# Performance work log

Measured on AMD Instinct MI355X. Metric: run time of the kernel, lower is better.

## Reference

```python
import jax, jax.numpy as jnp
import numpy as np

D_MODEL = 1024
NUM_HEADS = 16
HEAD_DIM = D_MODEL // NUM_HEADS


def setup_inputs() -> dict:
    key = jax.random.key(0)
    ks = jax.random.split(key, 9)
    B, S = 4, 2048
    scale = 1.0 / np.sqrt(D_MODEL)
    x = jax.random.normal(ks[0], (B, S, D_MODEL), dtype=jnp.float32)
    Wq = jax.random.normal(ks[1], (D_MODEL, D_MODEL), dtype=jnp.float32) * scale
    bq = jnp.zeros((D_MODEL,), dtype=jnp.float32)
    Wk = jax.random.normal(ks[2], (D_MODEL, D_MODEL), dtype=jnp.float32) * scale
    bk = jnp.zeros((D_MODEL,), dtype=jnp.float32)
    Wv = jax.random.normal(ks[3], (D_MODEL, D_MODEL), dtype=jnp.float32) * scale
    bv = jnp.zeros((D_MODEL,), dtype=jnp.float32)
    Wo = jax.random.normal(ks[4], (D_MODEL, D_MODEL), dtype=jnp.float32) * scale
    bo = jnp.zeros((D_MODEL,), dtype=jnp.float32)
    return {"x": x, "Wq": Wq, "bq": bq, "Wk": Wk, "bk": bk,
            "Wv": Wv, "bv": bv, "Wo": Wo, "bo": bo}


def reference(x, Wq, bq, Wk, bk, Wv, bv, Wo, bo):
    B, S, D = x.shape
    H, Hd = NUM_HEADS, HEAD_DIM
    # linear projections then split heads: [B,S,D] -> [B,H,S,Hd]
    def split(t):
        return t.reshape(B, S, H, Hd).transpose(0, 2, 1, 3)
    q = split(x @ Wq + bq)
    k = split(x @ Wk + bk)
    v = split(x @ Wv + bv)
    scores = jnp.einsum('bhsd,bhtd->bhst', q, k) / jnp.sqrt(
        jnp.asarray(Hd, dtype=jnp.float32))
    attn = jax.nn.softmax(scores, axis=-1)
    out = jnp.einsum('bhst,bhtd->bhsd', attn, v)  # [B,H,S,Hd]
    out = out.transpose(0, 2, 1, 3).reshape(B, S, D)
    return out @ Wo + bo
```

## Files before the change

kernel.cpp:

```cpp
#include <hip/hip_runtime.h>

#define DM 1024
#define NH 16
#define HD 64
#define SEQ 2048
#define BATCH 4
#define MROWS (BATCH*SEQ)

typedef short short8 __attribute__((ext_vector_type(8)));
typedef float f32x4 __attribute__((ext_vector_type(4)));
typedef unsigned short u16x8 __attribute__((ext_vector_type(8)));
typedef unsigned short u16x4 __attribute__((ext_vector_type(4)));

__device__ inline unsigned short f2b(float f) {
    union { float f; unsigned u; } v; v.f = f;
    unsigned r = v.u + 0x7fffu + ((v.u >> 16) & 1u);
    return (unsigned short)(r >> 16);
}

__device__ inline void gload_lds16(const void* g, void* l) {
    __builtin_amdgcn_global_load_lds(
        (const __attribute__((address_space(1))) void*)g,
        (__attribute__((address_space(3))) void*)l, 16, 0, 0);
}

__device__ inline unsigned cvt_pk_bf16(float lo, float hi) {
    unsigned r;
    asm("v_cvt_pk_bf16_f32 %0, %1, %2" : "=v"(r) : "v"(lo), "v"(hi));
    return r;
}

__global__ void k_cvt_x(const float* __restrict__ x, unsigned short* __restrict__ xb) {
    long i = ((long)blockIdx.x * 256 + threadIdx.x) * 8;
    float4 a = *reinterpret_cast<const float4*>(x + i);
    float4 b = *reinterpret_cast<const float4*>(x + i + 4);
    u16x8 o;
    o[0]=f2b(a.x); o[1]=f2b(a.y); o[2]=f2b(a.z); o[3]=f2b(a.w);
    o[4]=f2b(b.x); o[5]=f2b(b.y); o[6]=f2b(b.z); o[7]=f2b(b.w);
    *reinterpret_cast<u16x8*>(xb + i) = o;
}

__global__ void k_cvt_wT(const float* W0, const float* W1, const float* W2, const float* W3,
                         unsigned short* __restrict__ out) {
    const float* Ws[4] = {W0, W1, W2, W3};
    const float* W = Ws[blockIdx.z];
    unsigned short* o = out + (size_t)blockIdx.z * DM * DM;
    __shared__ float t[64][65];
    int tx = threadIdx.x & 15, ty = threadIdx.x >> 4;
    int nb = blockIdx.x * 64, kb = blockIdx.y * 64;
#pragma unroll
    for (int i = 0; i < 4; ++i) {
        int r = ty + 16 * i;
        float4 v = *reinterpret_cast<const float4*>(W + (size_t)(kb + r) * DM + nb + tx * 4);
        t[r][tx*4+0] = v.x; t[r][tx*4+1] = v.y; t[r][tx*4+2] = v.z; t[r][tx*4+3] = v.w;
    }
    __syncthreads();
#pragma unroll
    for (int i = 0; i < 4; ++i) {
        int r = ty + 16 * i;
        u16x4 pv;
#pragma unroll
        for (int j = 0; j < 4; ++j) pv[j] = f2b(t[tx*4+j][r]);
        *reinterpret_cast<u16x4*>(o + (size_t)(nb + r) * DM + kb + tx * 4) = pv;
    }
}

#define BM 128
#define BN 128
#define BK 64
#define QSCALE 0.1803368801f

__global__ __launch_bounds__(256) void k_gemm_qkv(const unsigned short* __restrict__ A,
                                                  const unsigned short* __restrict__ WT,
                                                  const float* __restrict__ bq,
                                                  const float* __restrict__ bk,
                                                  const float* __restrict__ bv,
                                                  unsigned short* __restrict__ Qb,
                                                  unsigned short* __restrict__ Kb,
                                                  unsigned short* __restrict__ VTb) {
    __shared__ unsigned short lds[BM*BK + BN*BK];
    unsigned short* lA = lds;
    unsigned short* lB = lds + BM*BK;
    int tid = threadIdx.x, lane = tid & 63, wv = tid >> 6;
    int wr = wv >> 1, wc = wv & 1;
    int c = lane & 15, g = lane >> 4;
    int m0 = blockIdx.x * BM, n0 = blockIdx.y * BN;
    f32x4 acc[4][4] = {};

    for (int kt = 0; kt < DM / BK; ++kt) {
#pragma unroll
        for (int it = 0; it < 4; ++it) {
            int sgi = it * 256 + tid;
            int row = sgi >> 3, blk = sgi & 7;
            int srcoff = kt * BK + ((blk ^ (row & 7)) << 3);
            gload_lds16(A  + (size_t)(m0 + row) * DM + srcoff, &lA[(it*256 + wv*64) * 8]);
            gload_lds16(WT + (size_t)(n0 + row) * DM + srcoff, &lB[(it*256 + wv*64) * 8]);
        }
        __syncthreads();
#pragma unroll
        for (int ks = 0; ks < 2; ++ks) {
            short8 af[4], bf[4];
#pragma unroll
            for (int mi = 0; mi < 4; ++mi) {
                int row = wr*64 + mi*16 + c;
                af[mi] = *reinterpret_cast<const short8*>(&lA[row*64 + (((ks*4 + g) ^ (row & 7)) << 3)]);
            }
#pragma unroll
            for (int ni = 0; ni < 4; ++ni) {
                int row = wc*64 + ni*16 + c;
                bf[ni] = *reinterpret_cast<const short8*>(&lB[row*64 + (((ks*4 + g) ^ (row & 7)) << 3)]);
            }
#pragma unroll
            for (int mi = 0; mi < 4; ++mi)
#pragma unroll
                for (int ni = 0; ni < 4; ++ni)
                    acc[mi][ni] = __builtin_amdgcn_mfma_f32_16x16x32_bf16(af[mi], bf[ni], acc[mi][ni], 0, 0, 0);
        }
        __syncthreads();
    }

    int mat = n0 >> 10;
    int gb = n0 & 1023;
    const float* bias = (mat == 0) ? bq : (mat == 1) ? bk : bv;

    if (mat < 2) {
        unsigned short* outb = (mat == 0) ? Qb : Kb;
        float sc = (mat == 0) ? QSCALE : 1.0f;
#pragma unroll
        for (int mi = 0; mi < 4; ++mi)
#pragma unroll
            for (int ni = 0; ni < 4; ++ni)
#pragma unroll
                for (int r = 0; r < 4; ++r) {
                    int gr = m0 + wr*64 + mi*16 + 4*g + r;
                    int gc = gb + wc*64 + ni*16 + c;
                    float v = (acc[mi][ni][r] + bias[gc]) * sc;
                    int b = gr >> 11, s = gr & 2047, h = gc >> 6, d = gc & 63;
                    outb[(((size_t)(b*NH + h) * SEQ + s) << 6) + d] = f2b(v);
                }
    } else {
        unsigned short* t = lds;
#pragma unroll
        for (int mi = 0; mi < 4; ++mi)
#pragma unroll
            for (int ni = 0; ni < 4; ++ni)
#pragma unroll
                for (int r = 0; r < 4; ++r) {
                    int lr = wr*64 + mi*16 + 4*g + r;
                    int lc = wc*64 + ni*16 + c;
                    t[lc*128 + lr] = f2b(acc[mi][ni][r] + bias[gb + lc]);
                }
        __syncthreads();
#pragma unroll
        for (int i = 0; i < 8; ++i) {
            int idx = (i*256 + tid) * 8;
            int lc = idx >> 7, lr = idx & 127;
            int gcol = gb + lc, grow = m0 + lr;
            int b = grow >> 11, s = grow & 2047, h = gcol >> 6, d = gcol & 63;
            *reinterpret_cast<u16x8*>(&VTb[((size_t)((b*NH + h) << 6) + d) * SEQ + s]) =
                *reinterpret_cast<u16x8*>(&t[idx]);
        }
    }
}

__global__ __launch_bounds__(256) void k_gemm_o(const unsigned short* __restrict__ A,
                                                const unsigned short* __restrict__ Bt,
                                                const float* __restrict__ bias,
                                                float* __restrict__ outf) {
    __shared__ unsigned short lds[BM*BK + BN*BK];
    unsigned short* lA = lds;
    unsigned short* lB = lds + BM*BK;
    int tid = threadIdx.x, lane = tid & 63, wv = tid >> 6;
    int wr = wv >> 1, wc = wv & 1;
    int c = lane & 15, g = lane >> 4;
    int m0 = blockIdx.x * BM, n0 = blockIdx.y * BN;
    f32x4 acc[4][4] = {};

    for (int kt = 0; kt < DM / BK; ++kt) {
#pragma unroll
        for (int it = 0; it < 4; ++it) {
            int sgi = it * 256 + tid;
            int row = sgi >> 3, blk = sgi & 7;
            int srcoff = kt * BK + ((blk ^ (row & 7)) << 3);
            gload_lds16(A  + (size_t)(m0 + row) * DM + srcoff, &lA[(it*256 + wv*64) * 8]);
            gload_lds16(Bt + (size_t)(n0 + row) * DM + srcoff, &lB[(it*256 + wv*64) * 8]);
        }
        __syncthreads();
#pragma unroll
        for (int ks = 0; ks < 2; ++ks) {
            short8 af[4], bf[4];
#pragma unroll
            for (int mi = 0; mi < 4; ++mi) {
                int row = wr*64 + mi*16 + c;
                af[mi] = *reinterpret_cast<const short8*>(&lA[row*64 + (((ks*4 + g) ^ (row & 7)) << 3)]);
            }
#pragma unroll
            for (int ni = 0; ni < 4; ++ni) {
                int row = wc*64 + ni*16 + c;
                bf[ni] = *reinterpret_cast<const short8*>(&lB[row*64 + (((ks*4 + g) ^ (row & 7)) << 3)]);
            }
#pragma unroll
            for (int mi = 0; mi < 4; ++mi)
#pragma unroll
                for (int ni = 0; ni < 4; ++ni)
                    acc[mi][ni] = __builtin_amdgcn_mfma_f32_16x16x32_bf16(af[mi], bf[ni], acc[mi][ni], 0, 0, 0);
        }
        __syncthreads();
    }

#pragma unroll
    for (int mi = 0; mi < 4; ++mi)
#pragma unroll
        for (int ni = 0; ni < 4; ++ni)
#pragma unroll
            for (int r = 0; r < 4; ++r) {
                int gr = m0 + wr*64 + mi*16 + 4*g + r;
                int gc = n0 + wc*64 + ni*16 + c;
                outf[(size_t)gr * DM + gc] = acc[mi][ni][r] + bias[gc];
            }
}

__global__ __launch_bounds__(256) void k_attn(const unsigned short* __restrict__ Q,
                                              const unsigned short* __restrict__ K,
                                              const unsigned short* __restrict__ VT,
                                              unsigned short* __restrict__ AO) {
    __shared__ unsigned short kt[2][64*64], vt[2][64*64];
    int tid = threadIdx.x, lane = tid & 63, wv = tid >> 6;
    int c = lane & 15, g = lane >> 4;

    int flat = blockIdx.x;
    int nb = (flat & 7) * 256 + (flat >> 3);
    int qb = nb & 31, bh = nb >> 5;

    const unsigned short* Qh = Q  + (size_t)bh * SEQ * HD;
    const unsigned short* Kh = K  + (size_t)bh * SEQ * HD;
    const unsigned short* Vh = VT + (size_t)bh * HD * SEQ;

    int qrow = qb*64 + wv*16 + c;
    short8 qf0 = *reinterpret_cast<const short8*>(&Qh[(size_t)qrow*HD +      g*8]);
    short8 qf1 = *reinterpret_cast<const short8*>(&Qh[(size_t)qrow*HD + 32 + g*8]);

    int row = tid >> 3, blk = tid & 7;
    int xo = (blk ^ (row & 7)) << 3;
    auto srowf = [](int r) {
        return ((r >> 4) & 1)*32 + ((r >> 2) & 3)*8 + ((r >> 5) & 1)*4 + (r & 3);
    };
    const unsigned short* gK0 = Kh + (size_t)srowf(row)      * HD + xo;
    const unsigned short* gK1 = Kh + (size_t)srowf(row + 32) * HD + xo;
    const unsigned short* gV0 = Vh + (size_t)row        * SEQ + xo;
    const unsigned short* gV1 = Vh + (size_t)(row + 32) * SEQ + xo;
    unsigned ldso = wv * 512;

    int swz0 = (g ^ (c & 7)) << 3;
    int swz1 = ((4 + g) ^ (c & 7)) << 3;
    const unsigned short* kb0 = &kt[0][c*64 + swz0];
    const unsigned short* kb1 = &kt[0][c*64 + swz1];
    const unsigned short* vb0 = &vt[0][c*64 + swz0];
    const unsigned short* vb1 = &vt[0][c*64 + swz1];

    float m = -1e30f;
    f32x4 oacc[4] = {}, lacc = {};
    const short ob = (short)0x3F80;
    const short8 ones = {ob, ob, ob, ob, ob, ob, ob, ob};

#define STAGE(SB) do {                                                        \
        gload_lds16(gK0, &kt[SB][ldso]);                                      \
        gload_lds16(gK1, &kt[SB][2048 + ldso]);                               \
        gload_lds16(gV0, &vt[SB][ldso]);                                      \
        gload_lds16(gV1, &vt[SB][2048 + ldso]);                               \
        gK0 += 64*HD; gK1 += 64*HD; gV0 += 64; gV1 += 64;                     \
    } while (0)

#define TILE(BUFO, PRE) do {                                                  \
        PRE;                                                                  \
        f32x4 sacc[4] = {};                                                   \
        __builtin_amdgcn_s_setprio(1);                                        \
        _Pragma("unroll")                                                     \
        for (int nt = 0; nt < 4; ++nt) {                                      \
            short8 kf0 = *reinterpret_cast<const short8*>(kb0 + (BUFO) + nt*1024); \
            short8 kf1 = *reinterpret_cast<const short8*>(kb1 + (BUFO) + nt*1024); \
            sacc[nt] = __builtin_amdgcn_mfma_f32_16x16x32_bf16(kf0, qf0, sacc[nt], 0, 0, 0); \
            sacc[nt] = __builtin_amdgcn_mfma_f32_16x16x32_bf16(kf1, qf1, sacc[nt], 0, 0, 0); \
        }                                                                     \
        __builtin_amdgcn_s_setprio(0);                                        \
        float x0 = fmaxf(fmaxf(sacc[0][0], sacc[0][1]), sacc[0][2]);          \
        float x1 = fmaxf(fmaxf(sacc[0][3], sacc[1][0]), sacc[1][1]);          \
        float x2 = fmaxf(fmaxf(sacc[1][2], sacc[1][3]), sacc[2][0]);          \
        float x3 = fmaxf(fmaxf(sacc[2][1], sacc[2][2]), sacc[2][3]);          \
        float x4 = fmaxf(fmaxf(sacc[3][0], sacc[3][1]), sacc[3][2]);          \
        float tm = fmaxf(fmaxf(fmaxf(x0, x1), fmaxf(x2, x3)), fmaxf(x4, sacc[3][3])); \
        if (__any(tm > m + 8.0f)) {                                           \
            tm = fmaxf(tm, __shfl_xor(tm, 16, 64));                           \
            tm = fmaxf(tm, __shfl_xor(tm, 32, 64));                           \
            float mn = fmaxf(m, tm);                                          \
            float corr = __builtin_amdgcn_exp2f(m - mn);                      \
            m = mn; lacc *= corr;                                             \
            _Pragma("unroll")                                                 \
            for (int ft = 0; ft < 4; ++ft)                                    \
                _Pragma("unroll")                                             \
                for (int r = 0; r < 4; ++r) oacc[ft][r] *= corr;              \
        }                                                                     \
        _Pragma("unroll")                                                     \
        for (int nt = 0; nt < 4; ++nt)                                        \
            _Pragma("unroll")                                                 \
            for (int r = 0; r < 4; ++r)                                       \
                sacc[nt][r] = __builtin_amdgcn_exp2f(sacc[nt][r] - m);        \
        union { unsigned u[4]; short8 v; } U0, U1;                            \
        U0.u[0] = cvt_pk_bf16(sacc[0][0], sacc[0][1]);                        \
        U0.u[1] = cvt_pk_bf16(sacc[0][2], sacc[0][3]);                        \
        U0.u[2] = cvt_pk_bf16(sacc[2][0], sacc[2][1]);                        \
        U0.u[3] = cvt_pk_bf16(sacc[2][2], sacc[2][3]);                        \
        U1.u[0] = cvt_pk_bf16(sacc[1][0], sacc[1][1]);                        \
        U1.u[1] = cvt_pk_bf16(sacc[1][2], sacc[1][3]);                        \
        U1.u[2] = cvt_pk_bf16(sacc[3][0], sacc[3][1]);                        \
        U1.u[3] = cvt_pk_bf16(sacc[3][2], sacc[3][3]);                        \
        short8 pa0 = U0.v, pa1 = U1.v;                                        \
        __builtin_amdgcn_s_setprio(1);                                        \
        _Pragma("unroll")                                                     \
        for (int ft = 0; ft < 4; ++ft) {                                      \
            short8 vf0 = *reinterpret_cast<const short8*>(vb0 + (BUFO) + ft*1024); \
            short8 vf1 = *reinterpret_cast<const short8*>(vb1 + (BUFO) + ft*1024); \
            oacc[ft] = __builtin_amdgcn_mfma_f32_16x16x32_bf16(vf0, pa0, oacc[ft], 0, 0, 0); \
            oacc[ft] = __builtin_amdgcn_mfma_f32_16x16x32_bf16(vf1, pa1, oacc[ft], 0, 0, 0); \
        }                                                                     \
        lacc = __builtin_amdgcn_mfma_f32_16x16x32_bf16(ones, pa0, lacc, 0, 0, 0); \
        lacc = __builtin_amdgcn_mfma_f32_16x16x32_bf16(ones, pa1, lacc, 0, 0, 0); \
        __builtin_amdgcn_s_setprio(0);                                        \
        __syncthreads();                                                      \
    } while (0)

    STAGE(0);
    __syncthreads();

    for (int tp = 0; tp < 15; ++tp) {
        TILE(0,    STAGE(1));
        TILE(4096, STAGE(0));
    }
    TILE(0,    STAGE(1));
    TILE(4096, (void)0);

#undef STAGE
#undef TILE

    int b = bh >> 4, h = bh & 15;
    float inv = 1.f / lacc[0];
#pragma unroll
    for (int ft = 0; ft < 4; ++ft) {
        u16x4 o4;
#pragma unroll
        for (int r = 0; r < 4; ++r) o4[r] = f2b(oacc[ft][r] * inv);
        *reinterpret_cast<u16x4*>(
            &AO[(size_t)(b*SEQ + qrow) * DM + h*HD + ft*16 + 4*g]) = o4;
    }
}

extern "C" void kernel_launch(void* const* d_in, const int* in_sizes, int n_in,
                              void* d_out, int out_size, void* d_ws, size_t ws_size,
                              hipStream_t stream) {
    const float* x  = (const float*)d_in[0];
    const float* Wq = (const float*)d_in[1];
    const float* bq = (const float*)d_in[2];
    const float* Wk = (const float*)d_in[3];
    const float* bk = (const float*)d_in[4];
    const float* Wv = (const float*)d_in[5];
    const float* bv = (const float*)d_in[6];
    const float* Wo = (const float*)d_in[7];
    const float* bo = (const float*)d_in[8];

    char* ws = (char*)d_ws;
    unsigned short* xb  = (unsigned short*)(ws);
    unsigned short* wT  = (unsigned short*)(ws + (16u<<20));
    unsigned short* Qb  = (unsigned short*)(ws + (24u<<20));
    unsigned short* Kb  = (unsigned short*)(ws + (40u<<20));
    unsigned short* VTb = (unsigned short*)(ws + (56u<<20));
    unsigned short* AOb = (unsigned short*)(ws + (72u<<20));

    k_cvt_x<<<dim3(MROWS*DM/8/256), 256, 0, stream>>>(x, xb);
    k_cvt_wT<<<dim3(16,16,4), 256, 0, stream>>>(Wq, Wk, Wv, Wo, wT);

    k_gemm_qkv<<<dim3(MROWS/BM, 3*DM/BN), 256, 0, stream>>>(xb, wT, bq, bk, bv, Qb, Kb, VTb);

    k_attn<<<dim3(SEQ/64 * BATCH*NH), 256, 0, stream>>>(Qb, Kb, VTb, AOb);

    k_gemm_o<<<dim3(MROWS/BM, DM/BN), 256, 0, stream>>>(AOb, wT + 3*DM*DM, bo, (float*)d_out);
}
```

Measured before the change: 199.6 us.

## Switch attention to 32x32x16 MFMA with 128-query blocks per workgroup

Rewrites the attention kernel to use 32x32x16 bf16 MFMAs, so each wave handles 32 query rows and the workgroup covers 128 queries. This halves the number of workgroups and the K/V tile loads per query. The P fragment for the PV MFMA is built with v_permlane32_swap, and the K staging drops the old row permutation in favour of an XOR-swizzled direct layout. In exchange it uses more accumulator registers per wave, which may cut occupancy, and relies on tricky fragment-layout correctness.

```diff
diff --git a/kernel.cpp b/kernel.cpp
--- a/kernel.cpp
+++ b/kernel.cpp
@@ -9,6 +9,7 @@
 
 typedef short short8 __attribute__((ext_vector_type(8)));
 typedef float f32x4 __attribute__((ext_vector_type(4)));
+typedef float f32x16 __attribute__((ext_vector_type(16)));
 typedef unsigned short u16x8 __attribute__((ext_vector_type(8)));
 typedef unsigned short u16x4 __attribute__((ext_vector_type(4)));
 
@@ -224,107 +225,127 @@
                                               const unsigned short* __restrict__ K,
                                               const unsigned short* __restrict__ VT,
                                               unsigned short* __restrict__ AO) {
-    __shared__ unsigned short kt[2][64*64], vt[2][64*64];
+    __shared__ unsigned short sm[4][64*64];
     int tid = threadIdx.x, lane = tid & 63, wv = tid >> 6;
-    int c = lane & 15, g = lane >> 4;
+    int q5 = lane & 31, hi = lane >> 5;
 
     int flat = blockIdx.x;
-    int nb = (flat & 7) * 256 + (flat >> 3);
-    int qb = nb & 31, bh = nb >> 5;
+    int nb = (flat & 7) * 128 + (flat >> 3);
+    int qb = nb & 15, bh = nb >> 4;
 
     const unsigned short* Qh = Q  + (size_t)bh * SEQ * HD;
     const unsigned short* Kh = K  + (size_t)bh * SEQ * HD;
     const unsigned short* Vh = VT + (size_t)bh * HD * SEQ;
 
-    int qrow = qb*64 + wv*16 + c;
-    short8 qf0 = *reinterpret_cast<const short8*>(&Qh[(size_t)qrow*HD +      g*8]);
-    short8 qf1 = *reinterpret_cast<const short8*>(&Qh[(size_t)qrow*HD + 32 + g*8]);
+    int qrow = qb*128 + wv*32 + q5;
+    short8 qf0 = *reinterpret_cast<const short8*>(&Qh[(size_t)qrow*HD +  0 + hi*8]);
+    short8 qf1 = *reinterpret_cast<const short8*>(&Qh[(size_t)qrow*HD + 16 + hi*8]);
+    short8 qf2 = *reinterpret_cast<const short8*>(&Qh[(size_t)qrow*HD + 32 + hi*8]);
+    short8 qf3 = *reinterpret_cast<const short8*>(&Qh[(size_t)qrow*HD + 48 + hi*8]);
 
     int row = tid >> 3, blk = tid & 7;
     int xo = (blk ^ (row & 7)) << 3;
-    auto srowf = [](int r) {
-        return ((r >> 4) & 1)*32 + ((r >> 2) & 3)*8 + ((r >> 5) & 1)*4 + (r & 3);
-    };
-    const unsigned short* gK0 = Kh + (size_t)srowf(row)      * HD + xo;
-    const unsigned short* gK1 = Kh + (size_t)srowf(row + 32) * HD + xo;
+    const unsigned short* gK0 = Kh + (size_t)row        * HD + xo;
+    const unsigned short* gK1 = Kh + (size_t)(row + 32) * HD + xo;
     const unsigned short* gV0 = Vh + (size_t)row        * SEQ + xo;
     const unsigned short* gV1 = Vh + (size_t)(row + 32) * SEQ + xo;
     unsigned ldso = wv * 512;
 
-    int swz0 = (g ^ (c & 7)) << 3;
-    int swz1 = ((4 + g) ^ (c & 7)) << 3;
-    const unsigned short* kb0 = &kt[0][c*64 + swz0];
-    const unsigned short* kb1 = &kt[0][c*64 + swz1];
-    const unsigned short* vb0 = &vt[0][c*64 + swz0];
-    const unsigned short* vb1 = &vt[0][c*64 + swz1];
+    const char* P0; const char* P1; const char* P2; const char* P3;
+    {
+        int o0 = (hi ^ (q5 & 7)) << 4;
+        const char* base = (const char*)&sm[0][0] + q5*128;
+        P0 = base + (o0 ^ 0);
+        P1 = base + (o0 ^ 32);
+        P2 = base + (o0 ^ 64);
+        P3 = base + (o0 ^ 96);
+    }
 
     float m = -1e30f;
-    f32x4 oacc[4] = {}, lacc = {};
+    f32x16 o0acc = {}, o1acc = {}, lacc = {};
     const short ob = (short)0x3F80;
     const short8 ones = {ob, ob, ob, ob, ob, ob, ob, ob};
 
 #define STAGE(SB) do {                                                        \
-        gload_lds16(gK0, &kt[SB][ldso]);                                      \
-        gload_lds16(gK1, &kt[SB][2048 + ldso]);                               \
-        gload_lds16(gV0, &vt[SB][ldso]);                                      \
-        gload_lds16(gV1, &vt[SB][2048 + ldso]);                               \
+        gload_lds16(gK0, &sm[SB][ldso]);                                      \
+        gload_lds16(gK1, &sm[SB][2048 + ldso]);                               \
+        gload_lds16(gV0, &sm[2 + (SB)][ldso]);                                \
+        gload_lds16(gV1, &sm[2 + (SB)][2048 + ldso]);                         \
         gK0 += 64*HD; gK1 += 64*HD; gV0 += 64; gV1 += 64;                     \
     } while (0)
 
+#define RD8(P, OFF) (*reinterpret_cast<const short8*>((P) + (OFF)))
+
+#define MKFRAG(F, SLO0, SLO1, SLO2, SLO3, SHI0, SHI1, SHI2, SHI3) do {        \
+        unsigned a0 = cvt_pk_bf16(SLO0, SLO1);                                \
+        unsigned b0 = cvt_pk_bf16(SHI0, SHI1);                                \
+        asm("v_permlane32_swap_b32 %0, %1" : "+v"(a0), "+v"(b0));             \
+        F.u[0] = a0; F.u[2] = b0;                                             \
+        unsigned a1 = cvt_pk_bf16(SLO2, SLO3);                                \
+        unsigned b1 = cvt_pk_bf16(SHI2, SHI3);                                \
+        asm("v_permlane32_swap_b32 %0, %1" : "+v"(a1), "+v"(b1));             \
+        F.u[1] = a1; F.u[3] = b1;                                             \
+    } while (0)
+
 #define TILE(BUFO, PRE) do {                                                  \
         PRE;                                                                  \
-        f32x4 sacc[4] = {};                                                   \
+        f32x16 s0 = {}, s1 = {};                                              \
         __builtin_amdgcn_s_setprio(1);                                        \
-        _Pragma("unroll")                                                     \
-        for (int nt = 0; nt < 4; ++nt) {                                      \
-            short8 kf0 = *reinterpret_cast<const short8*>(kb0 + (BUFO) + nt*1024); \
-            short8 kf1 = *reinterpret_cast<const short8*>(kb1 + (BUFO) + nt*1024); \
-            sacc[nt] = __builtin_amdgcn_mfma_f32_16x16x32_bf16(kf0, qf0, sacc[nt], 0, 0, 0); \
-            sacc[nt] = __builtin_amdgcn_mfma_f32_16x16x32_bf16(kf1, qf1, sacc[nt], 0, 0, 0); \
-        }                                                                     \
+        s0 = __builtin_amdgcn_mfma_f32_32x32x16_bf16(RD8(P0, BUFO),      qf0, s0, 0, 0, 0); \
+        s1 = __builtin_amdgcn_mfma_f32_32x32x16_bf16(RD8(P0, BUFO+4096), qf0, s1, 0, 0, 0); \
+        s0 = __builtin_amdgcn_mfma_f32_32x32x16_bf16(RD8(P1, BUFO),      qf1, s0, 0, 0, 0); \
+        s1 = __builtin_amdgcn_mfma_f32_32x32x16_bf16(RD8(P1, BUFO+4096), qf1, s1, 0, 0, 0); \
+        s0 = __builtin_amdgcn_mfma_f32_32x32x16_bf16(RD8(P2, BUFO),      qf2, s0, 0, 0, 0); \
+        s1 = __builtin_amdgcn_mfma_f32_32x32x16_bf16(RD8(P2, BUFO+4096), qf2, s1, 0, 0, 0); \
+        s0 = __builtin_amdgcn_mfma_f32_32x32x16_bf16(RD8(P3, BUFO),      qf3, s0, 0, 0, 0); \
+        s1 = __builtin_amdgcn_mfma_f32_32x32x16_bf16(RD8(P3, BUFO+4096), qf3, s1, 0, 0, 0); \
         __builtin_amdgcn_s_setprio(0);                                        \
-        float x0 = fmaxf(fmaxf(sacc[0][0], sacc[0][1]), sacc[0][2]);          \
-        float x1 = fmaxf(fmaxf(sacc[0][3], sacc[1][0]), sacc[1][1]);          \
-        float x2 = fmaxf(fmaxf(sacc[1][2], sacc[1][3]), sacc[2][0]);          \
-        float x3 = fmaxf(fmaxf(sacc[2][1], sacc[2][2]), sacc[2][3]);          \
-        float x4 = fmaxf(fmaxf(sacc[3][0], sacc[3][1]), sacc[3][2]);          \
-        float tm = fmaxf(fmaxf(fmaxf(x0, x1), fmaxf(x2, x3)), fmaxf(x4, sacc[3][3])); \
+        float x0 = fmaxf(fmaxf(s0[0],  s0[1]),  s0[2]);                       \
+        float x1 = fmaxf(fmaxf(s0[3],  s0[4]),  s0[5]);                       \
+        float x2 = fmaxf(fmaxf(s0[6],  s0[7]),  s0[8]);                       \
+        float x3 = fmaxf(fmaxf(s0[9],  s0[10]), s0[11]);                      \
+        float x4 = fmaxf(fmaxf(s0[12], s0[13]), s0[14]);                      \
+        float x5 = fmaxf(fmaxf(s0[15], s1[0]),  s1[1]);                       \
+        float x6 = fmaxf(fmaxf(s1[2],  s1[3]),  s1[4]);                       \
+        float x7 = fmaxf(fmaxf(s1[5],  s1[6]),  s1[7]);                       \
+        float x8 = fmaxf(fmaxf(s1[8],  s1[9]),  s1[10]);                      \
+        float x9 = fmaxf(fmaxf(s1[11], s1[12]), s1[13]);                      \
+        float y  = fmaxf(s1[14], s1[15]);                                     \
+        float z0 = fmaxf(fmaxf(x0, x1), x2);                                  \
+        float z1 = fmaxf(fmaxf(x3, x4), x5);                                  \
+        float z2 = fmaxf(fmaxf(x6, x7), x8);                                  \
+        float tm = fmaxf(fmaxf(fmaxf(z0, z1), z2), fmaxf(x9, y));             \
         if (__any(tm > m + 8.0f)) {                                           \
-            tm = fmaxf(tm, __shfl_xor(tm, 16, 64));                           \
-            tm = fmaxf(tm, __shfl_xor(tm, 32, 64));                           \
-            float mn = fmaxf(m, tm);                                          \
+            float fl = fmaxf(tm, __shfl_xor(tm, 32, 64));                     \
+            float mn = fmaxf(m, fl);                                          \
             float corr = __builtin_amdgcn_exp2f(m - mn);                      \
-            m = mn; lacc *= corr;                                             \
+            m = mn; lacc[0] *= corr;                                          \
             _Pragma("unroll")                                                 \
-            for (int ft = 0; ft < 4; ++ft)                                    \
-                _Pragma("unroll")                                             \
-                for (int r = 0; r < 4; ++r) oacc[ft][r] *= corr;              \
+            for (int r = 0; r < 16; ++r) { o0acc[r] *= corr; o1acc[r] *= corr; } \
         }                                                                     \
         _Pragma("unroll")                                                     \
-        for (int nt = 0; nt < 4; ++nt)                                        \
-            _Pragma("unroll")                                                 \
-            for (int r = 0; r < 4; ++r)                                       \
-                sacc[nt][r] = __builtin_amdgcn_exp2f(sacc[nt][r] - m);        \
-        union { unsigned u[4]; short8 v; } U0, U1;                            \
-        U0.u[0] = cvt_pk_bf16(sacc[0][0], sacc[0][1]);                        \
-        U0.u[1] = cvt_pk_bf16(sacc[0][2], sacc[0][3]);                        \
-        U0.u[2] = cvt_pk_bf16(sacc[2][0], sacc[2][1]);                        \
-        U0.u[3] = cvt_pk_bf16(sacc[2][2], sacc[2][3]);                        \
-        U1.u[0] = cvt_pk_bf16(sacc[1][0], sacc[1][1]);                        \
-        U1.u[1] = cvt_pk_bf16(sacc[1][2], sacc[1][3]);                        \
-        U1.u[2] = cvt_pk_bf16(sacc[3][0], sacc[3][1]);                        \
-        U1.u[3] = cvt_pk_bf16(sacc[3][2], sacc[3][3]);                        \
-        short8 pa0 = U0.v, pa1 = U1.v;                                        \
+        for (int r = 0; r < 16; ++r) {                                        \
+            s0[r] = __builtin_amdgcn_exp2f(s0[r] - m);                        \
+            s1[r] = __builtin_amdgcn_exp2f(s1[r] - m);                        \
+        }                                                                     \
+        union { unsigned u[4]; short8 v; } F0, F1, F2, F3;                    \
+        MKFRAG(F0, s0[0],  s0[1],  s0[2],  s0[3],  s0[4],  s0[5],  s0[6],  s0[7]);  \
+        MKFRAG(F1, s0[8],  s0[9],  s0[10], s0[11], s0[12], s0[13], s0[14], s0[15]); \
+        MKFRAG(F2, s1[0],  s1[1],  s1[2],  s1[3],  s1[4],  s1[5],  s1[6],  s1[7]);  \
+        MKFRAG(F3, s1[8],  s1[9],  s1[10], s1[11], s1[12], s1[13], s1[14], s1[15]); \
         __builtin_amdgcn_s_setprio(1);                                        \
-        _Pragma("unroll")                                                     \
-        for (int ft = 0; ft < 4; ++ft) {                                      \
-            short8 vf0 = *reinterpret_cast<const short8*>(vb0 + (BUFO) + ft*1024); \
-            short8 vf1 = *reinterpret_cast<const short8*>(vb1 + (BUFO) + ft*1024); \
-            oacc[ft] = __builtin_amdgcn_mfma_f32_16x16x32_bf16(vf0, pa0, oacc[ft], 0, 0, 0); \
-            oacc[ft] = __builtin_amdgcn_mfma_f32_16x16x32_bf16(vf1, pa1, oacc[ft], 0, 0, 0); \
-        }                                                                     \
-        lacc = __builtin_amdgcn_mfma_f32_16x16x32_bf16(ones, pa0, lacc, 0, 0, 0); \
-        lacc = __builtin_amdgcn_mfma_f32_16x16x32_bf16(ones, pa1, lacc, 0, 0, 0); \
+        o0acc = __builtin_amdgcn_mfma_f32_32x32x16_bf16(RD8(P0, 16384+BUFO),      F0.v, o0acc, 0, 0, 0); \
+        o1acc = __builtin_amdgcn_mfma_f32_32x32x16_bf16(RD8(P0, 16384+BUFO+4096), F0.v, o1acc, 0, 0, 0); \
+        lacc  = __builtin_amdgcn_mfma_f32_32x32x16_bf16(ones, F0.v, lacc, 0, 0, 0); \
+        o0acc = __builtin_amdgcn_mfma_f32_32x32x16_bf16(RD8(P1, 16384+BUFO),      F1.v, o0acc, 0, 0, 0); \
+        o1acc = __builtin_amdgcn_mfma_f32_32x32x16_bf16(RD8(P1, 16384+BUFO+4096), F1.v, o1acc, 0, 0, 0); \
+        lacc  = __builtin_amdgcn_mfma_f32_32x32x16_bf16(ones, F1.v, lacc, 0, 0, 0); \
+        o0acc = __builtin_amdgcn_mfma_f32_32x32x16_bf16(RD8(P2, 16384+BUFO),      F2.v, o0acc, 0, 0, 0); \
+        o1acc = __builtin_amdgcn_mfma_f32_32x32x16_bf16(RD8(P2, 16384+BUFO+4096), F2.v, o1acc, 0, 0, 0); \
+        lacc  = __builtin_amdgcn_mfma_f32_32x32x16_bf16(ones, F2.v, lacc, 0, 0, 0); \
+        o0acc = __builtin_amdgcn_mfma_f32_32x32x16_bf16(RD8(P3, 16384+BUFO),      F3.v, o0acc, 0, 0, 0); \
+        o1acc = __builtin_amdgcn_mfma_f32_32x32x16_bf16(RD8(P3, 16384+BUFO+4096), F3.v, o1acc, 0, 0, 0); \
+        lacc  = __builtin_amdgcn_mfma_f32_32x32x16_bf16(ones, F3.v, lacc, 0, 0, 0); \
         __builtin_amdgcn_s_setprio(0);                                        \
         __syncthreads();                                                      \
     } while (0)
@@ -334,23 +355,29 @@
 
     for (int tp = 0; tp < 15; ++tp) {
         TILE(0,    STAGE(1));
-        TILE(4096, STAGE(0));
+        TILE(8192, STAGE(0));
     }
     TILE(0,    STAGE(1));
-    TILE(4096, (void)0);
+    TILE(8192, (void)0);
 
 #undef STAGE
 #undef TILE
+#undef RD8
+#undef MKFRAG
 
     int b = bh >> 4, h = bh & 15;
     float inv = 1.f / lacc[0];
-#pragma unroll
-    for (int ft = 0; ft < 4; ++ft) {
-        u16x4 o4;
-#pragma unroll
-        for (int r = 0; r < 4; ++r) o4[r] = f2b(oacc[ft][r] * inv);
-        *reinterpret_cast<u16x4*>(
-            &AO[(size_t)(b*SEQ + qrow) * DM + h*HD + ft*16 + 4*g]) = o4;
+    unsigned short* aob = &AO[(size_t)(b*SEQ + qrow) * DM + h*HD];
+#pragma unroll
+    for (int rg = 0; rg < 4; ++rg) {
+        u16x4 oa, obv;
+#pragma unroll
+        for (int j = 0; j < 4; ++j) {
+            oa[j]  = f2b(o0acc[rg*4 + j] * inv);
+            obv[j] = f2b(o1acc[rg*4 + j] * inv);
+        }
+        *reinterpret_cast<u16x4*>(aob + rg*8 + hi*4)      = oa;
+        *reinterpret_cast<u16x4*>(aob + 32 + rg*8 + hi*4) = obv;
     }
 }
 
@@ -380,7 +407,7 @@
 
     k_gemm_qkv<<<dim3(MROWS/BM, 3*DM/BN), 256, 0, stream>>>(xb, wT, bq, bk, bv, Qb, Kb, VTb);
 
-    k_attn<<<dim3(SEQ/64 * BATCH*NH), 256, 0, stream>>>(Qb, Kb, VTb, AOb);
+    k_attn<<<dim3(SEQ/128 * BATCH*NH), 256, 0, stream>>>(Qb, Kb, VTb, AOb);
 
     k_gemm_o<<<dim3(MROWS/BM, DM/BN), 256, 0, stream>>>(AOb, wT + 3*DM*DM, bo, (float*)d_out);
 }
```

Measured after the change: 197.7 us. No clear change (-1.0%).

## Add double-buffered 256x256 GEMM kernel for Q/K and output projections

Applied to the files above, without the earlier changes.

Adds a new 512-thread GEMM kernel with 256x256 tiles, double-buffered LDS staging with explicit vmcnt waits, s_setprio around MFMA bursts, and XCD-aware block swizzling. It is used for the Q/K projection and the output projection. The V projection stays on the old 128x128 kernel, now launched separately because it needs the transposed epilogue. The larger tiles raise data reuse and overlap loads with compute. In exchange the grids are smaller (256 and 128 blocks), which may underfill the GPU's compute units, and there is one extra launch.

```diff
diff --git a/kernel.cpp b/kernel.cpp
--- a/kernel.cpp
+++ b/kernel.cpp
@@ -70,14 +70,11 @@
 #define BK 64
 #define QSCALE 0.1803368801f
 
-__global__ __launch_bounds__(256) void k_gemm_qkv(const unsigned short* __restrict__ A,
-                                                  const unsigned short* __restrict__ WT,
-                                                  const float* __restrict__ bq,
-                                                  const float* __restrict__ bk,
-                                                  const float* __restrict__ bv,
-                                                  unsigned short* __restrict__ Qb,
-                                                  unsigned short* __restrict__ Kb,
-                                                  unsigned short* __restrict__ VTb) {
+__global__ __launch_bounds__(256) void k_gemm(const unsigned short* __restrict__ A,
+                                              const unsigned short* __restrict__ Bt,
+                                              const float* __restrict__ bias,
+                                              unsigned short* __restrict__ outb,
+                                              float* __restrict__ outf, int mode) {
     __shared__ unsigned short lds[BM*BK + BN*BK];
     unsigned short* lA = lds;
     unsigned short* lB = lds + BM*BK;
@@ -94,7 +91,7 @@
             int row = sgi >> 3, blk = sgi & 7;
             int srcoff = kt * BK + ((blk ^ (row & 7)) << 3);
             gload_lds16(A  + (size_t)(m0 + row) * DM + srcoff, &lA[(it*256 + wv*64) * 8]);
-            gload_lds16(WT + (size_t)(n0 + row) * DM + srcoff, &lB[(it*256 + wv*64) * 8]);
+            gload_lds16(Bt + (size_t)(n0 + row) * DM + srcoff, &lB[(it*256 + wv*64) * 8]);
         }
         __syncthreads();
 #pragma unroll
@@ -119,105 +116,172 @@
         __syncthreads();
     }
 
-    int mat = n0 >> 10;
-    int gb = n0 & 1023;
-    const float* bias = (mat == 0) ? bq : (mat == 1) ? bk : bv;
-
-    if (mat < 2) {
-        unsigned short* outb = (mat == 0) ? Qb : Kb;
-        float sc = (mat == 0) ? QSCALE : 1.0f;
+    if (mode == 2) {
+        unsigned short* t = lds;
 #pragma unroll
         for (int mi = 0; mi < 4; ++mi)
 #pragma unroll
             for (int ni = 0; ni < 4; ++ni)
 #pragma unroll
                 for (int r = 0; r < 4; ++r) {
-                    int gr = m0 + wr*64 + mi*16 + 4*g + r;
-                    int gc = gb + wc*64 + ni*16 + c;
-                    float v = (acc[mi][ni][r] + bias[gc]) * sc;
-                    int b = gr >> 11, s = gr & 2047, h = gc >> 6, d = gc & 63;
+                    int lr = wr*64 + mi*16 + 4*g + r;
+                    int lc = wc*64 + ni*16 + c;
+                    t[lc*128 + lr] = f2b(acc[mi][ni][r] + bias[n0 + lc]);
+                }
+        __syncthreads();
+#pragma unroll
+        for (int i = 0; i < 8; ++i) {
+            int idx = (i*256 + tid) * 8;
+            int lc = idx >> 7, lr = idx & 127;
+            int gcol = n0 + lc, grow = m0 + lr;
+            int b = grow >> 11, s = grow & 2047, h = gcol >> 6, d = gcol & 63;
+            *reinterpret_cast<u16x8*>(&outb[((size_t)((b*NH + h) << 6) + d) * SEQ + s]) =
+                *reinterpret_cast<u16x8*>(&t[idx]);
+        }
+    }
+}
+
+__global__ __launch_bounds__(512, 2) void k_gemm256(const unsigned short* __restrict__ A,
+                                                    const unsigned short* __restrict__ Bt,
+                                                    const float* __restrict__ b0,
+                                                    const float* __restrict__ b1,
+                                                    unsigned short* __restrict__ oQ,
+                                                    unsigned short* __restrict__ oK,
+                                                    float* __restrict__ oF,
+                                                    int perXcd, int mode) {
+    __shared__ unsigned short L[2][2][2][128*64];
+    int tid = threadIdx.x, lane = tid & 63, wid = tid >> 6;
+    int wm = wid >> 2, wn = wid & 3;
+    int c = lane & 15, g = lane >> 4;
+
+    int bid = blockIdx.x;
+    int swz = (bid & 7) * perXcd + (bid >> 3);
+    int mb = swz & 31, nb = swz >> 5;
+    int m0 = mb * 256, n0 = nb * 256;
+
+    int idx0 = tid, idx1 = 512 + tid;
+    int r0 = idx0 >> 3, k0 = idx0 & 7;
+    int r1 = idx1 >> 3, k1 = idx1 & 7;
+
+    auto stageHalf = [&](int buf, int ab, int half, int kt) {
+        const unsigned short* src = ab ? Bt : A;
+        int base = (ab ? n0 : m0) + half * 128;
+        gload_lds16(src + (size_t)(base + r0) * DM + kt*64 + ((k0 ^ (r0 & 7)) << 3),
+                    &L[buf][ab][half][idx0 * 8]);
+        gload_lds16(src + (size_t)(base + r1) * DM + kt*64 + ((k1 ^ (r1 & 7)) << 3),
+                    &L[buf][ab][half][idx1 * 8]);
+    };
+
+    f32x4 acc[8][4] = {};
+    short8 af[4][2], bf0[2][2], bf1[2][2];
+
+    stageHalf(0, 0, 0, 0); stageHalf(0, 1, 0, 0);
+    stageHalf(0, 0, 1, 0); stageHalf(0, 1, 1, 0);
+
+#define RDA(BUF, I, MH, KS) (*reinterpret_cast<const short8*>(                         \
+        &L[BUF][0][wm][((MH)*64 + (I)*16 + c)*64 +                                     \
+                       ((((KS)*4 + g) ^ (((MH)*64 + (I)*16 + c) & 7)) << 3)]))
+#define RDB(BUF, J, NHh, KS) (*reinterpret_cast<const short8*>(                        \
+        &L[BUF][1][wn>>1][((wn&1)*64 + (NHh)*32 + (J)*16 + c)*64 +                     \
+                       ((((KS)*4 + g) ^ (((wn&1)*64 + (NHh)*32 + (J)*16 + c) & 7)) << 3)]))
+
+    for (int it = 0; it < 16; ++it) {
+        int cur = it & 1, nxt = cur ^ 1;
+
+        if (it < 15) {
+            stageHalf(nxt, 0, 0, it+1); stageHalf(nxt, 1, 0, it+1);
+            stageHalf(nxt, 0, 1, it+1); stageHalf(nxt, 1, 1, it+1);
+            asm volatile("s_waitcnt vmcnt(8)" ::: "memory");
+        } else {
+            asm volatile("s_waitcnt vmcnt(0)" ::: "memory");
+        }
+        __builtin_amdgcn_s_barrier();
+
+#pragma unroll
+        for (int i = 0; i < 4; ++i) { af[i][0] = RDA(cur, i, 0, 0); af[i][1] = RDA(cur, i, 0, 1); }
+#pragma unroll
+        for (int j = 0; j < 2; ++j) { bf0[j][0] = RDB(cur, j, 0, 0); bf0[j][1] = RDB(cur, j, 0, 1); }
+        __builtin_amdgcn_s_setprio(1);
+#pragma unroll
+        for (int i = 0; i < 4; ++i)
+#pragma unroll
+            for (int j = 0; j < 2; ++j) {
+                acc[i][j] = __builtin_amdgcn_mfma_f32_16x16x32_bf16(af[i][0], bf0[j][0], acc[i][j], 0, 0, 0);
+                acc[i][j] = __builtin_amdgcn_mfma_f32_16x16x32_bf16(af[i][1], bf0[j][1], acc[i][j], 0, 0, 0);
+            }
+        __builtin_amdgcn_s_setprio(0);
+
+#pragma unroll
+        for (int i = 0; i < 4; ++i) { af[i][0] = RDA(cur, i, 1, 0); af[i][1] = RDA(cur, i, 1, 1); }
+        __builtin_amdgcn_s_setprio(1);
+#pragma unroll
+        for (int i = 0; i < 4; ++i)
+#pragma unroll
+            for (int j = 0; j < 2; ++j) {
+                acc[4+i][j] = __builtin_amdgcn_mfma_f32_16x16x32_bf16(af[i][0], bf0[j][0], acc[4+i][j], 0, 0, 0);
+                acc[4+i][j] = __builtin_amdgcn_mfma_f32_16x16x32_bf16(af[i][1], bf0[j][1], acc[4+i][j], 0, 0, 0);
+            }
+        __builtin_amdgcn_s_setprio(0);
+
+#pragma unroll
+        for (int j = 0; j < 2; ++j) { bf1[j][0] = RDB(cur, j, 1, 0); bf1[j][1] = RDB(cur, j, 1, 1); }
+        __builtin_amdgcn_s_setprio(1);
+#pragma unroll
+        for (int i = 0; i < 4; ++i)
+#pragma unroll
+            for (int j = 0; j < 2; ++j) {
+                acc[4+i][2+j] = __builtin_amdgcn_mfma_f32_16x16x32_bf16(af[i][0], bf1[j][0], acc[4+i][2+j], 0, 0, 0);
+                acc[4+i][2+j] = __builtin_amdgcn_mfma_f32_16x16x32_bf16(af[i][1], bf1[j][1], acc[4+i][2+j], 0, 0, 0);
+            }
+        __builtin_amdgcn_s_setprio(0);
+
+#pragma unroll
+        for (int i = 0; i < 4; ++i) { af[i][0] = RDA(cur, i, 0, 0); af[i][1] = RDA(cur, i, 0, 1); }
+        __builtin_amdgcn_s_setprio(1);
+#pragma unroll
+        for (int i = 0; i < 4; ++i)
+#pragma unroll
+            for (int j = 0; j < 2; ++j) {
+                acc[i][2+j] = __builtin_amdgcn_mfma_f32_16x16x32_bf16(af[i][0], bf1[j][0], acc[i][2+j], 0, 0, 0);
+                acc[i][2+j] = __builtin_amdgcn_mfma_f32_16x16x32_bf16(af[i][1], bf1[j][1], acc[i][2+j], 0, 0, 0);
+            }
+        __builtin_amdgcn_s_setprio(0);
+
+        __builtin_amdgcn_s_barrier();
+    }
+#undef RDA
+#undef RDB
+
+    if (mode == 0) {
+        int mat = n0 >> 10;
+        const float* bias = mat ? b1 : b0;
+        unsigned short* outb = mat ? oK : oQ;
+        float sc = mat ? 1.0f : QSCALE;
+#pragma unroll
+        for (int mf = 0; mf < 8; ++mf)
+#pragma unroll
+            for (int nf = 0; nf < 4; ++nf)
+#pragma unroll
+                for (int r = 0; r < 4; ++r) {
+                    int gr = m0 + wm*128 + mf*16 + 4*g + r;
+                    int gc = n0 + wn*64 + nf*16 + c;
+                    int gcm = gc & 1023;
+                    float v = (acc[mf][nf][r] + bias[gcm]) * sc;
+                    int b = gr >> 11, s = gr & 2047, h = gcm >> 6, d = gcm & 63;
                     outb[(((size_t)(b*NH + h) * SEQ + s) << 6) + d] = f2b(v);
                 }
     } else {
-        unsigned short* t = lds;
-#pragma unroll
-        for (int mi = 0; mi < 4; ++mi)
-#pragma unroll
-            for (int ni = 0; ni < 4; ++ni)
+#pragma unroll
+        for (int mf = 0; mf < 8; ++mf)
+#pragma unroll
+            for (int nf = 0; nf < 4; ++nf)
 #pragma unroll
                 for (int r = 0; r < 4; ++r) {
-                    int lr = wr*64 + mi*16 + 4*g + r;
-                    int lc = wc*64 + ni*16 + c;
-                    t[lc*128 + lr] = f2b(acc[mi][ni][r] + bias[gb + lc]);
+                    int gr = m0 + wm*128 + mf*16 + 4*g + r;
+                    int gc = n0 + wn*64 + nf*16 + c;
+                    oF[(size_t)gr * DM + gc] = acc[mf][nf][r] + b0[gc];
                 }
-        __syncthreads();
-#pragma unroll
-        for (int i = 0; i < 8; ++i) {
-            int idx = (i*256 + tid) * 8;
-            int lc = idx >> 7, lr = idx & 127;
-            int gcol = gb + lc, grow = m0 + lr;
-            int b = grow >> 11, s = grow & 2047, h = gcol >> 6, d = gcol & 63;
-            *reinterpret_cast<u16x8*>(&VTb[((size_t)((b*NH + h) << 6) + d) * SEQ + s]) =
-                *reinterpret_cast<u16x8*>(&t[idx]);
-        }
-    }
-}
-
-__global__ __launch_bounds__(256) void k_gemm_o(const unsigned short* __restrict__ A,
-                                                const unsigned short* __restrict__ Bt,
-                                                const float* __restrict__ bias,
-                                                float* __restrict__ outf) {
-    __shared__ unsigned short lds[BM*BK + BN*BK];
-    unsigned short* lA = lds;
-    unsigned short* lB = lds + BM*BK;
-    int tid = threadIdx.x, lane = tid & 63, wv = tid >> 6;
-    int wr = wv >> 1, wc = wv & 1;
-    int c = lane & 15, g = lane >> 4;
-    int m0 = blockIdx.x * BM, n0 = blockIdx.y * BN;
-    f32x4 acc[4][4] = {};
-
-    for (int kt = 0; kt < DM / BK; ++kt) {
-#pragma unroll
-        for (int it = 0; it < 4; ++it) {
-            int sgi = it * 256 + tid;
-            int row = sgi >> 3, blk = sgi & 7;
-            int srcoff = kt * BK + ((blk ^ (row & 7)) << 3);
-            gload_lds16(A  + (size_t)(m0 + row) * DM + srcoff, &lA[(it*256 + wv*64) * 8]);
-            gload_lds16(Bt + (size_t)(n0 + row) * DM + srcoff, &lB[(it*256 + wv*64) * 8]);
-        }
-        __syncthreads();
-#pragma unroll
-        for (int ks = 0; ks < 2; ++ks) {
-            short8 af[4], bf[4];
-#pragma unroll
-            for (int mi = 0; mi < 4; ++mi) {
-                int row = wr*64 + mi*16 + c;
-                af[mi] = *reinterpret_cast<const short8*>(&lA[row*64 + (((ks*4 + g) ^ (row & 7)) << 3)]);
-            }
-#pragma unroll
-            for (int ni = 0; ni < 4; ++ni) {
-                int row = wc*64 + ni*16 + c;
-                bf[ni] = *reinterpret_cast<const short8*>(&lB[row*64 + (((ks*4 + g) ^ (row & 7)) << 3)]);
-            }
-#pragma unroll
-            for (int mi = 0; mi < 4; ++mi)
-#pragma unroll
-                for (int ni = 0; ni < 4; ++ni)
-                    acc[mi][ni] = __builtin_amdgcn_mfma_f32_16x16x32_bf16(af[mi], bf[ni], acc[mi][ni], 0, 0, 0);
-        }
-        __syncthreads();
-    }
-
-#pragma unroll
-    for (int mi = 0; mi < 4; ++mi)
-#pragma unroll
-        for (int ni = 0; ni < 4; ++ni)
-#pragma unroll
-            for (int r = 0; r < 4; ++r) {
-                int gr = m0 + wr*64 + mi*16 + 4*g + r;
-                int gc = n0 + wc*64 + ni*16 + c;
-                outf[(size_t)gr * DM + gc] = acc[mi][ni][r] + bias[gc];
-            }
+    }
 }
 
 __global__ __launch_bounds__(256) void k_attn(const unsigned short* __restrict__ Q,
@@ -378,9 +442,12 @@
     k_cvt_x<<<dim3(MROWS*DM/8/256), 256, 0, stream>>>(x, xb);
     k_cvt_wT<<<dim3(16,16,4), 256, 0, stream>>>(Wq, Wk, Wv, Wo, wT);
 
-    k_gemm_qkv<<<dim3(MROWS/BM, 3*DM/BN), 256, 0, stream>>>(xb, wT, bq, bk, bv, Qb, Kb, VTb);
+    k_gemm256<<<dim3(256), 512, 0, stream>>>(xb, wT, bq, bk, Qb, Kb, nullptr, 32, 0);
+
+    k_gemm<<<dim3(MROWS/BM, DM/BN), 256, 0, stream>>>(xb, wT + 2*DM*DM, bv, VTb, nullptr, 2);
 
     k_attn<<<dim3(SEQ/64 * BATCH*NH), 256, 0, stream>>>(Qb, Kb, VTb, AOb);
 
-    k_gemm_o<<<dim3(MROWS/BM, DM/BN), 256, 0, stream>>>(AOb, wT + 3*DM*DM, bo, (float*)d_out);
-}
+    k_gemm256<<<dim3(128), 512, 0, stream>>>(AOb, wT + 3*DM*DM, bo, nullptr, nullptr, nullptr,
+                                             (float*)d_out, 16, 1);
+}
```

Result: slower. 207.1 us (+3.7%).
